# Optimization experiments

Hardware: AMD Instinct MI355X
Metric: run time of the kernel (lower is better)

Reference implementation:

```python
import jax, jax.numpy as jnp
import numpy as np

B, DIM, HEADS, H, W = 2, 256, 8, 40, 40


def setup_inputs() -> dict:
    key = jax.random.key(0)
    ks = jax.random.split(key, 11)
    s = 0.05
    return {
        "x": jax.random.normal(ks[0], (B, DIM, H, W), jnp.float32),
        "qkv_w": jax.random.normal(ks[1], (3 * DIM, DIM, 1, 1), jnp.float32) * s,
        "qkv_b": jax.random.normal(ks[2], (3 * DIM,), jnp.float32) * s,
        "pos_w": jax.random.normal(ks[3], (3 * DIM, 1, 3, 3), jnp.float32) * s,
        "pos_b": jax.random.normal(ks[4], (3 * DIM,), jnp.float32) * s,
        "proj_w": jax.random.normal(ks[5], (DIM, DIM), jnp.float32) * s,
        "proj_b": jax.random.normal(ks[6], (DIM,), jnp.float32) * s,
        "g1_w": jax.random.normal(ks[7], (16, 1), jnp.float32),
        "g1_b": jax.random.normal(ks[8], (16,), jnp.float32),
        "g2_w": jax.random.normal(ks[9], (1, 16), jnp.float32),
        "g2_b": jax.random.normal(ks[10], (1,), jnp.float32),
    }


def _conv(x, w, b, groups=1, pad=0):
    # NCHW conv, OIHW weights (matches torch Conv2d)
    y = jax.lax.conv_general_dilated(x, w, (1, 1), [(pad, pad), (pad, pad)],
                                     feature_group_count=groups)
    return y + b[None, :, None, None]


def reference(x, qkv_w, qkv_b, pos_w, pos_b, proj_w, proj_b, g1_w, g1_b, g2_w, g2_b):
    b, c, h, w = x.shape
    n = h * w
    hd = c // HEADS
    scale = hd ** -0.5

    qkv = _conv(x, qkv_w, qkv_b)                     # [b, 3c, h, w]
    qkv = _conv(qkv, pos_w, pos_b, groups=3 * c, pad=1)  # depthwise 3x3
    q, k, v = jnp.split(qkv, 3, axis=1)

    def to_heads(t):  # [b,c,h,w] -> [b, heads, n, head_dim]
        return t.reshape(b, HEADS, hd, n).transpose(0, 1, 3, 2)

    q, k, v = to_heads(q), to_heads(k), to_heads(v)

    attn = jnp.einsum('bhnd,bhmd->bhnm', q, k) * scale      # [b,H,n,n]
    prob = jax.nn.softmax(attn, axis=-1)
    entropy = -(prob * jnp.log(jnp.clip(prob, 1e-12))).sum(-1).mean(-1)  # [b,H]

    # EntropyGate: ratio in [0.1, 1.0]
    hid = jax.nn.relu(entropy[..., None] @ g1_w.T + g1_b)
    ratio = jax.nn.sigmoid(hid @ g2_w.T + g2_b)[..., 0] * 0.9 + 0.1      # [b,H]

    # dynamic per-(b,head) top-k: keep = ceil(ratio*n), clamped to [1,n]
    keep = jnp.clip(jnp.ceil(ratio * n).astype(jnp.int32), 1, n)          # [b,H]
    srt = jnp.flip(jnp.sort(attn, axis=-1), axis=-1)                      # descending
    idx = jnp.broadcast_to((keep - 1)[:, :, None, None], (b, HEADS, n, 1))
    kth = jnp.take_along_axis(srt, idx, axis=-1)                          # [b,H,n,1]
    sparse = jnp.where(attn >= kth, attn, -jnp.inf)

    p = jax.nn.softmax(sparse, axis=-1)
    out = jnp.einsum('bhnm,bhmd->bhnd', p, v)
    out = out.transpose(0, 2, 1, 3).reshape(b, n, c)
    out = out @ proj_w.T + proj_b
    return out.transpose(0, 2, 1).reshape(b, c, h, w)
```

## Files before the change

### kernel.cpp

```cpp
#include <hip/hip_runtime.h>
#include <math.h>

#define BB 2
#define CDIM 256
#define NHEADS 8
#define HD 32
#define HH 40
#define WW 40
#define NN 1600
#define C3 768
#define SCALE 0.17677669529663687f
#define RTE 8
#define RTS 2
#define TSTR 2048
#define HSTR 51200

__device__ inline unsigned fkey(float f) {
    unsigned u = __float_as_uint(f);
    return (u & 0x80000000u) ? ~u : (u | 0x80000000u);
}
__device__ inline float finv(unsigned u) {
    unsigned v = (u & 0x80000000u) ? (u ^ 0x80000000u) : ~u;
    return __uint_as_float(v);
}

__global__ __launch_bounds__(256) void conv1x1_kernel(const float* __restrict__ x,
                                                      const float* __restrict__ w,
                                                      const float* __restrict__ bias,
                                                      float* __restrict__ out) {
    int blk = blockIdx.x;
    int st = blk % 7;
    int t2 = blk / 7;
    int ocg = t2 % (C3 / 8);
    int b = t2 / (C3 / 8);
    int s = st * 256 + threadIdx.x;
    if (s >= NN) return;
    int oc0 = ocg * 8;
    const float* xb = x + (size_t)b * CDIM * NN + s;
    const float* w0 = w + (size_t)oc0 * CDIM;
    float a[8];
#pragma unroll
    for (int i = 0; i < 8; i++) a[i] = bias[oc0 + i];
#pragma unroll 4
    for (int ic = 0; ic < CDIM; ic++) {
        float xv = xb[(size_t)ic * NN];
#pragma unroll
        for (int i = 0; i < 8; i++) a[i] += w0[i * CDIM + ic] * xv;
    }
    float* ob = out + ((size_t)b * C3 + oc0) * NN + s;
#pragma unroll
    for (int i = 0; i < 8; i++) ob[(size_t)i * NN] = a[i];
}

__global__ __launch_bounds__(256) void dwconv_kernel(const float* __restrict__ in,
                                                     const float* __restrict__ w,
                                                     const float* __restrict__ bias,
                                                     float* __restrict__ out_t) {
    int idx = blockIdx.x * 256 + threadIdx.x;
    int s = idx % NN;
    int t = idx / NN;
    int c = t % C3;
    int b = t / C3;
    int y = s / WW, xx = s % WW;
    const float* ib = in + ((size_t)b * C3 + c) * NN;
    const float* wr = w + (size_t)c * 9;
    float acc = bias[c];
#pragma unroll
    for (int ky = 0; ky < 3; ky++) {
        int iy = y + ky - 1;
        if (iy < 0 || iy >= HH) continue;
#pragma unroll
        for (int kx = 0; kx < 3; kx++) {
            int ix = xx + kx - 1;
            if (ix < 0 || ix >= WW) continue;
            acc += wr[ky * 3 + kx] * ib[iy * WW + ix];
        }
    }
    int part = c >> 8;
    int r = c & 255;
    int hh = r >> 5;
    int d = r & 31;
    out_t[((size_t)(b * 3 + part) * NHEADS + hh) * HSTR + (s >> 6) * TSTR + d * 64 + (s & 63)] = acc;
}

__global__ __launch_bounds__(256) void entropy_kernel(const float* __restrict__ qkv_t,
                                                      float* __restrict__ ent) {
    int blk = blockIdx.x;
    int rt = blk % (NN / RTE);
    int bh = blk / (NN / RTE);
    int h = bh % NHEADS, b = bh / NHEADS;
    int row0 = rt * RTE;
    __shared__ float Qs[RTE][HD];
    int tid = threadIdx.x;
    const float* qt = qkv_t + ((size_t)(b * 3 + 0) * NHEADS + h) * HSTR;
    const float* ktb = qkv_t + ((size_t)(b * 3 + 1) * NHEADS + h) * HSTR;
    {
        int r = tid >> 5, d = tid & 31;
        int row = row0 + r;
        Qs[r][d] = qt[(row >> 6) * TSTR + d * 64 + (row & 63)];
    }
    __syncthreads();
    int w = tid >> 6, lane = tid & 63;
    int lr0 = 2 * w, lr1 = lr0 + 1;
    float q0[HD], q1[HD];
#pragma unroll
    for (int d = 0; d < HD; d++) { q0[d] = Qs[lr0][d]; q1[d] = Qs[lr1][d]; }
    float S0 = 0.f, T0 = 0.f, S1 = 0.f, T1 = 0.f;
#pragma unroll 1
    for (int kt = 0; kt < 25; kt++) {
        const float* kp = ktb + kt * TSTR + lane;
        float a0 = 0.f, a1 = 0.f;
#pragma unroll
        for (int dc = 0; dc < 4; dc++) {
            float kc[8];
#pragma unroll
            for (int i = 0; i < 8; i++) kc[i] = kp[(dc * 8 + i) * 64];
#pragma unroll
            for (int i = 0; i < 8; i++) {
                a0 += q0[dc * 8 + i] * kc[i];
                a1 += q1[dc * 8 + i] * kc[i];
            }
        }
        a0 *= SCALE; a1 *= SCALE;
        float e0 = __expf(a0), e1 = __expf(a1);
        S0 += e0; T0 += e0 * a0;
        S1 += e1; T1 += e1 * a1;
    }
#pragma unroll
    for (int o = 1; o < 64; o <<= 1) {
        S0 += __shfl_xor(S0, o); T0 += __shfl_xor(T0, o);
        S1 += __shfl_xor(S1, o); T1 += __shfl_xor(T1, o);
    }
    if (lane == 0) {
        ent[(size_t)bh * NN + row0 + lr0] = logf(S0) - T0 / S0;
        ent[(size_t)bh * NN + row0 + lr1] = logf(S1) - T1 / S1;
    }
}

__global__ void gate_kernel(const float* __restrict__ ent_rows,
                            const float* __restrict__ g1w, const float* __restrict__ g1b,
                            const float* __restrict__ g2w, const float* __restrict__ g2b,
                            int* __restrict__ keep) {
    int bh = blockIdx.x;
    int tid = threadIdx.x;
    __shared__ float red[4];
    float ls = 0.f;
    for (int j = tid; j < NN; j += 256) ls += ent_rows[bh * NN + j];
    for (int o = 32; o > 0; o >>= 1) ls += __shfl_down(ls, o);
    int lane = tid & 63, wid = tid >> 6;
    if (lane == 0) red[wid] = ls;
    __syncthreads();
    if (tid == 0) {
        float ent = (red[0] + red[1] + red[2] + red[3]) / (float)NN;
        float val = g2b[0];
#pragma unroll
        for (int j = 0; j < 16; j++) {
            float hid = ent * g1w[j] + g1b[j];
            if (hid < 0.f) hid = 0.f;
            val += hid * g2w[j];
        }
        float ratio = 0.9f / (1.f + expf(-val)) + 0.1f;
        int kp = (int)ceilf(ratio * (float)NN);
        if (kp < 1) kp = 1;
        if (kp > NN) kp = NN;
        keep[bh] = kp;
    }
}

__global__ __launch_bounds__(64) void sparse_attn_kernel(const float* __restrict__ qkv_t,
                                                         const int* __restrict__ keep,
                                                         float* __restrict__ oht) {
    int blk = blockIdx.x;
    int rt = blk % (NN / RTS);
    int bh = blk / (NN / RTS);
    int h = bh % NHEADS, b = bh / NHEADS;
    int row0 = rt * RTS;
    __shared__ float att[RTS][NN];
    __shared__ unsigned hist[RTS][256];
    __shared__ float Qs[RTS][HD];
    int tid = threadIdx.x;
    const float* qt = qkv_t + ((size_t)(b * 3 + 0) * NHEADS + h) * HSTR;
    const float* ktb = qkv_t + ((size_t)(b * 3 + 1) * NHEADS + h) * HSTR;
    const float* vtb = qkv_t + ((size_t)(b * 3 + 2) * NHEADS + h) * HSTR;
    {
        int r = tid >> 5, d = tid & 31;
        int row = row0 + r;
        Qs[r][d] = qt[(row >> 6) * TSTR + d * 64 + (row & 63)];
    }
    int want = keep[bh];
    __syncthreads();
    int lane = tid;
    float q0[HD], q1[HD];
#pragma unroll
    for (int d = 0; d < HD; d++) { q0[d] = Qs[0][d]; q1[d] = Qs[1][d]; }

    float m0 = -1e30f, m1 = -1e30f;
    for (int kt = 0; kt < 25; kt++) {
        const float* kp = ktb + kt * TSTR + lane;
        int j = kt * 64 + lane;
        float kc[HD];
#pragma unroll
        for (int d = 0; d < HD; d++) kc[d] = kp[d * 64];
        float a0 = 0.f, a1 = 0.f;
#pragma unroll
        for (int d = 0; d < HD; d++) { a0 += q0[d] * kc[d]; a1 += q1[d] * kc[d]; }
        a0 *= SCALE; a1 *= SCALE;
        att[0][j] = a0;
        att[1][j] = a1;
        m0 = fmaxf(m0, a0); m1 = fmaxf(m1, a1);
    }
#pragma unroll
    for (int off = 1; off < 64; off <<= 1) {
        m0 = fmaxf(m0, __shfl_xor(m0, off));
        m1 = fmaxf(m1, __shfl_xor(m1, off));
    }

    int l = lane & 31;
    int r = (lane < 32) ? 0 : 1;
    unsigned kvr[50];
#pragma unroll
    for (int k2 = 0; k2 < 50; k2++) kvr[k2] = fkey(att[r][k2 * 32 + l]);

    unsigned prefixHigh = 0;
    for (int pass = 0; pass < 4; pass++) {
        int shift = 24 - 8 * pass;
#pragma unroll
        for (int i = 0; i < 8; i++) hist[r][248 - 8 * l + i] = 0u;
#pragma unroll
        for (int k2 = 0; k2 < 50; k2++) {
            unsigned u = kvr[k2];
            bool ok = (pass == 0) || ((u >> (shift + 8)) == prefixHigh);
            if (ok) atomicAdd(&hist[r][(u >> shift) & 255u], 1u);
        }
        unsigned sch = 0;
#pragma unroll
        for (int i = 0; i < 8; i++) sch += hist[r][248 - 8 * l + i];
        unsigned inc = sch;
#pragma unroll
        for (int dlt = 1; dlt < 32; dlt <<= 1) {
            unsigned tv = __shfl_up(inc, dlt, 32);
            if (l >= dlt) inc += tv;
        }
        unsigned pref = inc - sch;
        bool found = (pref < (unsigned)want) && ((unsigned)want <= inc);
        int bsel = -1, wnew = 0;
        if (found) {
            unsigned want2 = (unsigned)want - pref, cum = 0;
#pragma unroll
            for (int i = 0; i < 8; i++) {
                int bbin = 255 - 8 * l - i;
                unsigned c = hist[r][bbin];
                if (bsel < 0 && cum + c >= want2) { bsel = bbin; wnew = (int)(want2 - cum); }
                cum += c;
            }
        }
        unsigned long long mk = __ballot(found);
        int src = (lane < 32) ? __builtin_ctzll(mk & 0xffffffffULL)
                              : __builtin_ctzll(mk >> 32) + 32;
        bsel = __shfl(bsel, src);
        want = __shfl(wnew, src);
        prefixHigh = (prefixHigh << 8) | (unsigned)bsel;
    }
    float kth = finv(prefixHigh);
    float kth0 = __shfl(kth, 0);
    float kth1 = __shfl(kth, 32);

    float acc0[HD], acc1[HD];
#pragma unroll
    for (int d = 0; d < HD; d++) { acc0[d] = 0.f; acc1[d] = 0.f; }
    float S0 = 0.f, S1 = 0.f;
    for (int kt = 0; kt < 25; kt++) {
        const float* vp = vtb + kt * TSTR + lane;
        int j = kt * 64 + lane;
        float a0 = att[0][j];
        float a1 = att[1][j];
        float p0 = (a0 >= kth0) ? __expf(a0 - m0) : 0.f;
        float p1 = (a1 >= kth1) ? __expf(a1 - m1) : 0.f;
        S0 += p0; S1 += p1;
#pragma unroll
        for (int d = 0; d < HD; d++) {
            float vv = vp[d * 64];
            acc0[d] += p0 * vv;
            acc1[d] += p1 * vv;
        }
    }
#pragma unroll
    for (int off = 1; off < 64; off <<= 1) {
        S0 += __shfl_xor(S0, off);
        S1 += __shfl_xor(S1, off);
    }

    float* scratch = &att[0][0];
    int dd = lane & 31;
    int jb = (lane < 32) ? 0 : 32;
#pragma unroll
    for (int d = 0; d < HD; d++) scratch[lane * 33 + d] = acc0[d];
    float sum0 = 0.f;
#pragma unroll
    for (int jj = 0; jj < 32; jj++) sum0 += scratch[(jb + jj) * 33 + dd];
    sum0 += __shfl_xor(sum0, 32);
#pragma unroll
    for (int d = 0; d < HD; d++) scratch[lane * 33 + d] = acc1[d];
    float sum1 = 0.f;
#pragma unroll
    for (int jj = 0; jj < 32; jj++) sum1 += scratch[(jb + jj) * 33 + dd];
    sum1 += __shfl_xor(sum1, 32);

    if (lane < 32) {
        size_t base = ((size_t)b * CDIM + h * HD + dd) * NN + row0;
        oht[base + 0] = sum0 / S0;
        oht[base + 1] = sum1 / S1;
    }
}

__global__ __launch_bounds__(256) void proj_kernel(const float* __restrict__ oht,
                                                   const float* __restrict__ pw,
                                                   const float* __restrict__ pb,
                                                   float* __restrict__ out) {
    int blk = blockIdx.x;
    int st = blk % 7;
    int t2 = blk / 7;
    int ocg = t2 % (CDIM / 8);
    int b = t2 / (CDIM / 8);
    int s = st * 256 + threadIdx.x;
    if (s >= NN) return;
    int co0 = ocg * 8;
    const float* ib = oht + (size_t)b * CDIM * NN + s;
    const float* w0 = pw + (size_t)co0 * CDIM;
    float a[8];
#pragma unroll
    for (int i = 0; i < 8; i++) a[i] = pb[co0 + i];
#pragma unroll 4
    for (int c = 0; c < CDIM; c++) {
        float xv = ib[(size_t)c * NN];
#pragma unroll
        for (int i = 0; i < 8; i++) a[i] += w0[i * CDIM + c] * xv;
    }
    float* ob = out + ((size_t)b * CDIM + co0) * NN + s;
#pragma unroll
    for (int i = 0; i < 8; i++) ob[(size_t)i * NN] = a[i];
}

extern "C" void kernel_launch(void* const* d_in, const int* in_sizes, int n_in,
                              void* d_out, int out_size, void* d_ws, size_t ws_size,
                              hipStream_t stream) {
    const float* x      = (const float*)d_in[0];
    const float* qkv_w  = (const float*)d_in[1];
    const float* qkv_b  = (const float*)d_in[2];
    const float* pos_w  = (const float*)d_in[3];
    const float* pos_b  = (const float*)d_in[4];
    const float* proj_w = (const float*)d_in[5];
    const float* proj_b = (const float*)d_in[6];
    const float* g1w    = (const float*)d_in[7];
    const float* g1b    = (const float*)d_in[8];
    const float* g2w    = (const float*)d_in[9];
    const float* g2b    = (const float*)d_in[10];
    float* out = (float*)d_out;

    float* ws   = (float*)d_ws;
    float* buf1 = ws;
    float* buf2 = buf1 + (size_t)BB * C3 * NN;
    float* ent  = buf2 + (size_t)BB * C3 * NN;
    float* oht  = ent + (size_t)BB * NHEADS * NN;
    int* keep   = (int*)(oht + (size_t)BB * CDIM * NN);

    conv1x1_kernel<<<BB * (C3 / 8) * 7, 256, 0, stream>>>(x, qkv_w, qkv_b, buf1);
    dwconv_kernel<<<BB * C3 * NN / 256, 256, 0, stream>>>(buf1, pos_w, pos_b, buf2);
    entropy_kernel<<<NHEADS * BB * (NN / RTE), 256, 0, stream>>>(buf2, ent);
    gate_kernel<<<BB * NHEADS, 256, 0, stream>>>(ent, g1w, g1b, g2w, g2b, keep);
    sparse_attn_kernel<<<NHEADS * BB * (NN / RTS), 64, 0, stream>>>(buf2, keep, oht);
    proj_kernel<<<BB * (CDIM / 8) * 7, 256, 0, stream>>>(oht, proj_w, proj_b, out);
}
```

Before: 437.4 us.

## Process four query rows per sparse-attention block with double-buffered K/V loads

Each sparse-attention block now handles four query rows instead of two, so every K and V tile loaded from global memory is reused across twice as many rows and the grid is halved. K and V tile loads are double-buffered in registers so the next tile's loads are issued while the current tile is computed. The radix top-k selection runs in two rounds over row pairs, reusing the existing histogram layout. Costs are much higher register pressure (four accumulator arrays plus two tile buffers), more shared memory per block, and lower occupancy.

```diff
diff --git a/kernel.cpp b/kernel.cpp
--- a/kernel.cpp
+++ b/kernel.cpp
@@ -11,7 +11,7 @@
 #define C3 768
 #define SCALE 0.17677669529663687f
 #define RTE 8
-#define RTS 2
+#define RTS4 4
 #define TSTR 2048
 #define HSTR 51200
 
@@ -167,127 +167,181 @@
     }
 }
 
+
+#define QKT_STEP(KT, CUR, NXT)                                                 \
+    {                                                                          \
+        int ktn = ((KT) + 1 < 25) ? (KT) + 1 : 24;                             \
+        const float* kq = ktb + ktn * TSTR + lane;                             \
+        _Pragma("unroll")                                                      \
+        for (int d = 0; d < HD; d++) NXT[d] = kq[d * 64];                      \
+        float a0 = 0.f, a1 = 0.f, a2 = 0.f, a3 = 0.f;                          \
+        _Pragma("unroll")                                                      \
+        for (int d = 0; d < HD; d++) {                                         \
+            float kv = CUR[d];                                                 \
+            a0 += q0[d] * kv; a1 += q1[d] * kv;                                \
+            a2 += q2[d] * kv; a3 += q3[d] * kv;                                \
+        }                                                                      \
+        a0 *= SCALE; a1 *= SCALE; a2 *= SCALE; a3 *= SCALE;                    \
+        int j = (KT) * 64 + lane;                                              \
+        att[0][j] = a0; att[1][j] = a1; att[2][j] = a2; att[3][j] = a3;        \
+        m0 = fmaxf(m0, a0); m1 = fmaxf(m1, a1);                                \
+        m2 = fmaxf(m2, a2); m3 = fmaxf(m3, a3);                                \
+    }
+
+#define PV_STEP(KT, CUR, NXT)                                                  \
+    {                                                                          \
+        int ktn = ((KT) + 1 < 25) ? (KT) + 1 : 24;                             \
+        const float* vq = vtb + ktn * TSTR + lane;                             \
+        _Pragma("unroll")                                                      \
+        for (int d = 0; d < HD; d++) NXT[d] = vq[d * 64];                      \
+        int j = (KT) * 64 + lane;                                              \
+        float a0 = att[0][j], a1 = att[1][j], a2 = att[2][j], a3 = att[3][j];  \
+        float p0 = (a0 >= kth0) ? __expf(a0 - m0) : 0.f;                       \
+        float p1 = (a1 >= kth1) ? __expf(a1 - m1) : 0.f;                       \
+        float p2 = (a2 >= kth2) ? __expf(a2 - m2) : 0.f;                       \
+        float p3 = (a3 >= kth3) ? __expf(a3 - m3) : 0.f;                       \
+        S0 += p0; S1 += p1; S2 += p2; S3 += p3;                                \
+        _Pragma("unroll")                                                      \
+        for (int d = 0; d < HD; d++) {                                         \
+            float vv = CUR[d];                                                 \
+            acc0[d] += p0 * vv; acc1[d] += p1 * vv;                            \
+            acc2[d] += p2 * vv; acc3[d] += p3 * vv;                            \
+        }                                                                      \
+    }
+
 __global__ __launch_bounds__(64) void sparse_attn_kernel(const float* __restrict__ qkv_t,
                                                          const int* __restrict__ keep,
                                                          float* __restrict__ oht) {
     int blk = blockIdx.x;
-    int rt = blk % (NN / RTS);
-    int bh = blk / (NN / RTS);
+    int rt = blk % (NN / RTS4);
+    int bh = blk / (NN / RTS4);
     int h = bh % NHEADS, b = bh / NHEADS;
-    int row0 = rt * RTS;
-    __shared__ float att[RTS][NN];
-    __shared__ unsigned hist[RTS][256];
-    __shared__ float Qs[RTS][HD];
+    int row0 = rt * RTS4;
+    __shared__ float att[RTS4][NN];
+    __shared__ unsigned hist[2][256];
+    __shared__ float Qs[RTS4][HD];
     int tid = threadIdx.x;
     const float* qt = qkv_t + ((size_t)(b * 3 + 0) * NHEADS + h) * HSTR;
     const float* ktb = qkv_t + ((size_t)(b * 3 + 1) * NHEADS + h) * HSTR;
     const float* vtb = qkv_t + ((size_t)(b * 3 + 2) * NHEADS + h) * HSTR;
-    {
-        int r = tid >> 5, d = tid & 31;
+#pragma unroll
+    for (int i = tid; i < RTS4 * HD; i += 64) {
+        int r = i >> 5, d = i & 31;
         int row = row0 + r;
         Qs[r][d] = qt[(row >> 6) * TSTR + d * 64 + (row & 63)];
     }
-    int want = keep[bh];
+    int want0 = keep[bh];
     __syncthreads();
     int lane = tid;
-    float q0[HD], q1[HD];
-#pragma unroll
-    for (int d = 0; d < HD; d++) { q0[d] = Qs[0][d]; q1[d] = Qs[1][d]; }
-
-    float m0 = -1e30f, m1 = -1e30f;
-    for (int kt = 0; kt < 25; kt++) {
-        const float* kp = ktb + kt * TSTR + lane;
-        int j = kt * 64 + lane;
-        float kc[HD];
-#pragma unroll
-        for (int d = 0; d < HD; d++) kc[d] = kp[d * 64];
-        float a0 = 0.f, a1 = 0.f;
-#pragma unroll
-        for (int d = 0; d < HD; d++) { a0 += q0[d] * kc[d]; a1 += q1[d] * kc[d]; }
-        a0 *= SCALE; a1 *= SCALE;
-        att[0][j] = a0;
-        att[1][j] = a1;
-        m0 = fmaxf(m0, a0); m1 = fmaxf(m1, a1);
-    }
+    float q0[HD], q1[HD], q2[HD], q3[HD];
+#pragma unroll
+    for (int d = 0; d < HD; d++) {
+        q0[d] = Qs[0][d]; q1[d] = Qs[1][d]; q2[d] = Qs[2][d]; q3[d] = Qs[3][d];
+    }
+
+    float m0 = -1e30f, m1 = -1e30f, m2 = -1e30f, m3 = -1e30f;
+    float kcA[HD], kcB[HD];
+    {
+        const float* kp0 = ktb + lane;
+#pragma unroll
+        for (int d = 0; d < HD; d++) kcA[d] = kp0[d * 64];
+    }
+#pragma unroll 1
+    for (int kt = 0; kt < 24; kt += 2) {
+        QKT_STEP(kt, kcA, kcB);
+        QKT_STEP(kt + 1, kcB, kcA);
+    }
+    QKT_STEP(24, kcA, kcB);
 #pragma unroll
     for (int off = 1; off < 64; off <<= 1) {
         m0 = fmaxf(m0, __shfl_xor(m0, off));
         m1 = fmaxf(m1, __shfl_xor(m1, off));
+        m2 = fmaxf(m2, __shfl_xor(m2, off));
+        m3 = fmaxf(m3, __shfl_xor(m3, off));
     }
 
     int l = lane & 31;
-    int r = (lane < 32) ? 0 : 1;
-    unsigned kvr[50];
-#pragma unroll
-    for (int k2 = 0; k2 < 50; k2++) kvr[k2] = fkey(att[r][k2 * 32 + l]);
-
-    unsigned prefixHigh = 0;
-    for (int pass = 0; pass < 4; pass++) {
-        int shift = 24 - 8 * pass;
-#pragma unroll
-        for (int i = 0; i < 8; i++) hist[r][248 - 8 * l + i] = 0u;
-#pragma unroll
-        for (int k2 = 0; k2 < 50; k2++) {
-            unsigned u = kvr[k2];
-            bool ok = (pass == 0) || ((u >> (shift + 8)) == prefixHigh);
-            if (ok) atomicAdd(&hist[r][(u >> shift) & 255u], 1u);
+    int r = lane >> 5;
+    float kth0, kth1, kth2, kth3;
+#pragma unroll 1
+    for (int b2 = 0; b2 < 2; b2++) {
+        int rowr = 2 * b2 + r;
+        unsigned kvr[50];
+#pragma unroll
+        for (int k2 = 0; k2 < 50; k2++) kvr[k2] = fkey(att[rowr][k2 * 32 + l]);
+        int want = want0;
+        unsigned prefixHigh = 0;
+        for (int pass = 0; pass < 4; pass++) {
+            int shift = 24 - 8 * pass;
+#pragma unroll
+            for (int i = 0; i < 8; i++) hist[r][248 - 8 * l + i] = 0u;
+#pragma unroll
+            for (int k2 = 0; k2 < 50; k2++) {
+                unsigned u = kvr[k2];
+                bool ok = (pass == 0) || ((u >> (shift + 8)) == prefixHigh);
+                if (ok) atomicAdd(&hist[r][(u >> shift) & 255u], 1u);
+            }
+            unsigned sch = 0;
+#pragma unroll
+            for (int i = 0; i < 8; i++) sch += hist[r][248 - 8 * l + i];
+            unsigned inc = sch;
+#pragma unroll
+            for (int dlt = 1; dlt < 32; dlt <<= 1) {
+                unsigned tv = __shfl_up(inc, dlt, 32);
+                if (l >= dlt) inc += tv;
+            }
+            unsigned pref = inc - sch;
+            bool found = (pref < (unsigned)want) && ((unsigned)want <= inc);
+            int bsel = -1, wnew = 0;
+            if (found) {
+                unsigned want2 = (unsigned)want - pref, cum = 0;
+#pragma unroll
+                for (int i = 0; i < 8; i++) {
+                    int bbin = 255 - 8 * l - i;
+                    unsigned c = hist[r][bbin];
+                    if (bsel < 0 && cum + c >= want2) { bsel = bbin; wnew = (int)(want2 - cum); }
+                    cum += c;
+                }
+            }
+            unsigned long long mk = __ballot(found);
+            int src = (lane < 32) ? __builtin_ctzll(mk & 0xffffffffULL)
+                                  : __builtin_ctzll(mk >> 32) + 32;
+            bsel = __shfl(bsel, src);
+            want = __shfl(wnew, src);
+            prefixHigh = (prefixHigh << 8) | (unsigned)bsel;
         }
-        unsigned sch = 0;
-#pragma unroll
-        for (int i = 0; i < 8; i++) sch += hist[r][248 - 8 * l + i];
-        unsigned inc = sch;
-#pragma unroll
-        for (int dlt = 1; dlt < 32; dlt <<= 1) {
-            unsigned tv = __shfl_up(inc, dlt, 32);
-            if (l >= dlt) inc += tv;
+        float kth = finv(prefixHigh);
+        if (b2 == 0) {
+            kth0 = __shfl(kth, 0);
+            kth1 = __shfl(kth, 32);
+        } else {
+            kth2 = __shfl(kth, 0);
+            kth3 = __shfl(kth, 32);
         }
-        unsigned pref = inc - sch;
-        bool found = (pref < (unsigned)want) && ((unsigned)want <= inc);
-        int bsel = -1, wnew = 0;
-        if (found) {
-            unsigned want2 = (unsigned)want - pref, cum = 0;
-#pragma unroll
-            for (int i = 0; i < 8; i++) {
-                int bbin = 255 - 8 * l - i;
-                unsigned c = hist[r][bbin];
-                if (bsel < 0 && cum + c >= want2) { bsel = bbin; wnew = (int)(want2 - cum); }
-                cum += c;
-            }
-        }
-        unsigned long long mk = __ballot(found);
-        int src = (lane < 32) ? __builtin_ctzll(mk & 0xffffffffULL)
-                              : __builtin_ctzll(mk >> 32) + 32;
-        bsel = __shfl(bsel, src);
-        want = __shfl(wnew, src);
-        prefixHigh = (prefixHigh << 8) | (unsigned)bsel;
-    }
-    float kth = finv(prefixHigh);
-    float kth0 = __shfl(kth, 0);
-    float kth1 = __shfl(kth, 32);
-
-    float acc0[HD], acc1[HD];
-#pragma unroll
-    for (int d = 0; d < HD; d++) { acc0[d] = 0.f; acc1[d] = 0.f; }
-    float S0 = 0.f, S1 = 0.f;
-    for (int kt = 0; kt < 25; kt++) {
-        const float* vp = vtb + kt * TSTR + lane;
-        int j = kt * 64 + lane;
-        float a0 = att[0][j];
-        float a1 = att[1][j];
-        float p0 = (a0 >= kth0) ? __expf(a0 - m0) : 0.f;
-        float p1 = (a1 >= kth1) ? __expf(a1 - m1) : 0.f;
-        S0 += p0; S1 += p1;
-#pragma unroll
-        for (int d = 0; d < HD; d++) {
-            float vv = vp[d * 64];
-            acc0[d] += p0 * vv;
-            acc1[d] += p1 * vv;
-        }
-    }
+    }
+
+    float acc0[HD], acc1[HD], acc2[HD], acc3[HD];
+#pragma unroll
+    for (int d = 0; d < HD; d++) { acc0[d] = 0.f; acc1[d] = 0.f; acc2[d] = 0.f; acc3[d] = 0.f; }
+    float S0 = 0.f, S1 = 0.f, S2 = 0.f, S3 = 0.f;
+    float vcA[HD], vcB[HD];
+    {
+        const float* vp0 = vtb + lane;
+#pragma unroll
+        for (int d = 0; d < HD; d++) vcA[d] = vp0[d * 64];
+    }
+#pragma unroll 1
+    for (int kt = 0; kt < 24; kt += 2) {
+        PV_STEP(kt, vcA, vcB);
+        PV_STEP(kt + 1, vcB, vcA);
+    }
+    PV_STEP(24, vcA, vcB);
 #pragma unroll
     for (int off = 1; off < 64; off <<= 1) {
         S0 += __shfl_xor(S0, off);
         S1 += __shfl_xor(S1, off);
+        S2 += __shfl_xor(S2, off);
+        S3 += __shfl_xor(S3, off);
     }
 
     float* scratch = &att[0][0];
@@ -305,11 +359,25 @@
 #pragma unroll
     for (int jj = 0; jj < 32; jj++) sum1 += scratch[(jb + jj) * 33 + dd];
     sum1 += __shfl_xor(sum1, 32);
+#pragma unroll
+    for (int d = 0; d < HD; d++) scratch[lane * 33 + d] = acc2[d];
+    float sum2 = 0.f;
+#pragma unroll
+    for (int jj = 0; jj < 32; jj++) sum2 += scratch[(jb + jj) * 33 + dd];
+    sum2 += __shfl_xor(sum2, 32);
+#pragma unroll
+    for (int d = 0; d < HD; d++) scratch[lane * 33 + d] = acc3[d];
+    float sum3 = 0.f;
+#pragma unroll
+    for (int jj = 0; jj < 32; jj++) sum3 += scratch[(jb + jj) * 33 + dd];
+    sum3 += __shfl_xor(sum3, 32);
 
     if (lane < 32) {
         size_t base = ((size_t)b * CDIM + h * HD + dd) * NN + row0;
         oht[base + 0] = sum0 / S0;
         oht[base + 1] = sum1 / S1;
+        oht[base + 2] = sum2 / S2;
+        oht[base + 3] = sum3 / S3;
     }
 }
 
@@ -368,6 +436,6 @@
     dwconv_kernel<<<BB * C3 * NN / 256, 256, 0, stream>>>(buf1, pos_w, pos_b, buf2);
     entropy_kernel<<<NHEADS * BB * (NN / RTE), 256, 0, stream>>>(buf2, ent);
     gate_kernel<<<BB * NHEADS, 256, 0, stream>>>(ent, g1w, g1b, g2w, g2b, keep);
-    sparse_attn_kernel<<<NHEADS * BB * (NN / RTS), 64, 0, stream>>>(buf2, keep, oht);
+    sparse_attn_kernel<<<NHEADS * BB * (NN / RTS4), 64, 0, stream>>>(buf2, keep, oht);
     proj_kernel<<<BB * (CDIM / 8) * 7, 256, 0, stream>>>(oht, proj_w, proj_b, out);
 }
```

Result: slower. 459.3 us (+5.0%).

## Store Q/K/V tiles row-major per token and prefetch K/V with double buffering

Applied to the files above, without the earlier changes.

Changes the intermediate qkv tile layout from d-major to token-major with 32 contiguous floats per token. The entropy and sparse attention kernels can then load each key or value row as eight float4 vector loads instead of 32 strided scalar loads. The QK^T and PV loops in the sparse attention kernel are software-pipelined with two register buffers so the next tile's loads are in flight during the current tile's FMAs. The trade-offs are higher register pressure, and each lane now reads a 128-byte contiguous row, so a wavefront's accesses are no longer coalesced across lanes.

```diff
diff --git a/kernel.cpp b/kernel.cpp
--- a/kernel.cpp
+++ b/kernel.cpp
@@ -14,6 +14,8 @@
 #define RTS 2
 #define TSTR 2048
 #define HSTR 51200
+
+typedef __attribute__((ext_vector_type(4))) float f4;
 
 __device__ inline unsigned fkey(float f) {
     unsigned u = __float_as_uint(f);
@@ -80,7 +82,7 @@
     int r = c & 255;
     int hh = r >> 5;
     int d = r & 31;
-    out_t[((size_t)(b * 3 + part) * NHEADS + hh) * HSTR + (s >> 6) * TSTR + d * 64 + (s & 63)] = acc;
+    out_t[((size_t)(b * 3 + part) * NHEADS + hh) * HSTR + (s >> 6) * TSTR + (s & 63) * 32 + d] = acc;
 }
 
 __global__ __launch_bounds__(256) void entropy_kernel(const float* __restrict__ qkv_t,
@@ -97,7 +99,7 @@
     {
         int r = tid >> 5, d = tid & 31;
         int row = row0 + r;
-        Qs[r][d] = qt[(row >> 6) * TSTR + d * 64 + (row & 63)];
+        Qs[r][d] = qt[(row >> 6) * TSTR + (row & 63) * 32 + d];
     }
     __syncthreads();
     int w = tid >> 6, lane = tid & 63;
@@ -108,17 +110,18 @@
     float S0 = 0.f, T0 = 0.f, S1 = 0.f, T1 = 0.f;
 #pragma unroll 1
     for (int kt = 0; kt < 25; kt++) {
-        const float* kp = ktb + kt * TSTR + lane;
+        const f4* kp = (const f4*)(ktb + kt * TSTR + lane * 32);
+        f4 kc[8];
+#pragma unroll
+        for (int i = 0; i < 8; i++) kc[i] = kp[i];
         float a0 = 0.f, a1 = 0.f;
 #pragma unroll
-        for (int dc = 0; dc < 4; dc++) {
-            float kc[8];
-#pragma unroll
-            for (int i = 0; i < 8; i++) kc[i] = kp[(dc * 8 + i) * 64];
-#pragma unroll
-            for (int i = 0; i < 8; i++) {
-                a0 += q0[dc * 8 + i] * kc[i];
-                a1 += q1[dc * 8 + i] * kc[i];
+        for (int i = 0; i < 8; i++) {
+#pragma unroll
+            for (int c = 0; c < 4; c++) {
+                float kv = kc[i][c];
+                a0 += q0[i * 4 + c] * kv;
+                a1 += q1[i * 4 + c] * kv;
             }
         }
         a0 *= SCALE; a1 *= SCALE;
@@ -166,6 +169,51 @@
         keep[bh] = kp;
     }
 }
+
+
+#define QKT_STEP(KT, CUR, NXT)                                                 \
+    {                                                                          \
+        int ktn = ((KT) + 1 < 25) ? (KT) + 1 : 24;                             \
+        const f4* kq = (const f4*)(ktb + ktn * TSTR + lane * 32);              \
+        _Pragma("unroll")                                                      \
+        for (int i = 0; i < 8; i++) NXT[i] = kq[i];                            \
+        float a0 = 0.f, a1 = 0.f;                                              \
+        _Pragma("unroll")                                                      \
+        for (int i = 0; i < 8; i++) {                                          \
+            _Pragma("unroll")                                                  \
+            for (int c = 0; c < 4; c++) {                                      \
+                float kv = CUR[i][c];                                          \
+                a0 += q0[i * 4 + c] * kv;                                      \
+                a1 += q1[i * 4 + c] * kv;                                      \
+            }                                                                  \
+        }                                                                      \
+        a0 *= SCALE; a1 *= SCALE;                                              \
+        int j = (KT) * 64 + lane;                                              \
+        att[0][j] = a0; att[1][j] = a1;                                        \
+        m0 = fmaxf(m0, a0); m1 = fmaxf(m1, a1);                                \
+    }
+
+#define PV_STEP(KT, CUR, NXT)                                                  \
+    {                                                                          \
+        int ktn = ((KT) + 1 < 25) ? (KT) + 1 : 24;                             \
+        const f4* vq = (const f4*)(vtb + ktn * TSTR + lane * 32);              \
+        _Pragma("unroll")                                                      \
+        for (int i = 0; i < 8; i++) NXT[i] = vq[i];                            \
+        int j = (KT) * 64 + lane;                                              \
+        float a0 = att[0][j], a1 = att[1][j];                                  \
+        float p0 = (a0 >= kth0) ? __expf(a0 - m0) : 0.f;                       \
+        float p1 = (a1 >= kth1) ? __expf(a1 - m1) : 0.f;                       \
+        S0 += p0; S1 += p1;                                                    \
+        _Pragma("unroll")                                                      \
+        for (int i = 0; i < 8; i++) {                                          \
+            _Pragma("unroll")                                                  \
+            for (int c = 0; c < 4; c++) {                                      \
+                float vv = CUR[i][c];                                          \
+                acc0[i * 4 + c] += p0 * vv;                                    \
+                acc1[i * 4 + c] += p1 * vv;                                    \
+            }                                                                  \
+        }                                                                      \
+    }
 
 __global__ __launch_bounds__(64) void sparse_attn_kernel(const float* __restrict__ qkv_t,
                                                          const int* __restrict__ keep,
@@ -185,7 +233,7 @@
     {
         int r = tid >> 5, d = tid & 31;
         int row = row0 + r;
-        Qs[r][d] = qt[(row >> 6) * TSTR + d * 64 + (row & 63)];
+        Qs[r][d] = qt[(row >> 6) * TSTR + (row & 63) * 32 + d];
     }
     int want = keep[bh];
     __syncthreads();
@@ -195,20 +243,18 @@
     for (int d = 0; d < HD; d++) { q0[d] = Qs[0][d]; q1[d] = Qs[1][d]; }
 
     float m0 = -1e30f, m1 = -1e30f;
-    for (int kt = 0; kt < 25; kt++) {
-        const float* kp = ktb + kt * TSTR + lane;
-        int j = kt * 64 + lane;
-        float kc[HD];
-#pragma unroll
-        for (int d = 0; d < HD; d++) kc[d] = kp[d * 64];
-        float a0 = 0.f, a1 = 0.f;
-#pragma unroll
-        for (int d = 0; d < HD; d++) { a0 += q0[d] * kc[d]; a1 += q1[d] * kc[d]; }
-        a0 *= SCALE; a1 *= SCALE;
-        att[0][j] = a0;
-        att[1][j] = a1;
-        m0 = fmaxf(m0, a0); m1 = fmaxf(m1, a1);
-    }
+    f4 kcA[8], kcB[8];
+    {
+        const f4* kp0 = (const f4*)(ktb + lane * 32);
+#pragma unroll
+        for (int i = 0; i < 8; i++) kcA[i] = kp0[i];
+    }
+#pragma unroll 1
+    for (int kt = 0; kt < 24; kt += 2) {
+        QKT_STEP(kt, kcA, kcB);
+        QKT_STEP(kt + 1, kcB, kcA);
+    }
+    QKT_STEP(24, kcA, kcB);
 #pragma unroll
     for (int off = 1; off < 64; off <<= 1) {
         m0 = fmaxf(m0, __shfl_xor(m0, off));
@@ -269,21 +315,18 @@
 #pragma unroll
     for (int d = 0; d < HD; d++) { acc0[d] = 0.f; acc1[d] = 0.f; }
     float S0 = 0.f, S1 = 0.f;
-    for (int kt = 0; kt < 25; kt++) {
-        const float* vp = vtb + kt * TSTR + lane;
-        int j = kt * 64 + lane;
-        float a0 = att[0][j];
-        float a1 = att[1][j];
-        float p0 = (a0 >= kth0) ? __expf(a0 - m0) : 0.f;
-        float p1 = (a1 >= kth1) ? __expf(a1 - m1) : 0.f;
-        S0 += p0; S1 += p1;
-#pragma unroll
-        for (int d = 0; d < HD; d++) {
-            float vv = vp[d * 64];
-            acc0[d] += p0 * vv;
-            acc1[d] += p1 * vv;
-        }
-    }
+    f4 vcA[8], vcB[8];
+    {
+        const f4* vp0 = (const f4*)(vtb + lane * 32);
+#pragma unroll
+        for (int i = 0; i < 8; i++) vcA[i] = vp0[i];
+    }
+#pragma unroll 1
+    for (int kt = 0; kt < 24; kt += 2) {
+        PV_STEP(kt, vcA, vcB);
+        PV_STEP(kt + 1, vcB, vcA);
+    }
+    PV_STEP(24, vcA, vcB);
 #pragma unroll
     for (int off = 1; off < 64; off <<= 1) {
         S0 += __shfl_xor(S0, off);
```

Result: slower. 1.027 ms (+134.9%).

## Split sparse attention block across two wavefronts with per-row radix select

Applied to the files above, without the earlier changes.

Raises the sparse attention block from one to two wavefronts. Each wave handles half of the key tiles for QK and PV, and each wave runs the 4-pass radix top-k select for one query row with 64 lanes instead of 32. Partial max, sum and accumulators are combined through shared memory with extra barriers, and the output reduction now uses shuffles before a smaller shared-memory sum. The aim is more parallelism and latency hiding per block, at the cost of extra block-level synchronisation and cross-wave reductions.

```diff
diff --git a/kernel.cpp b/kernel.cpp
--- a/kernel.cpp
+++ b/kernel.cpp
@@ -167,9 +167,9 @@
     }
 }
 
-__global__ __launch_bounds__(64) void sparse_attn_kernel(const float* __restrict__ qkv_t,
-                                                         const int* __restrict__ keep,
-                                                         float* __restrict__ oht) {
+__global__ __launch_bounds__(128) void sparse_attn_kernel(const float* __restrict__ qkv_t,
+                                                          const int* __restrict__ keep,
+                                                          float* __restrict__ oht) {
     int blk = blockIdx.x;
     int rt = blk % (NN / RTS);
     int bh = blk / (NN / RTS);
@@ -178,33 +178,46 @@
     __shared__ float att[RTS][NN];
     __shared__ unsigned hist[RTS][256];
     __shared__ float Qs[RTS][HD];
+    __shared__ float red[RTS][2];
+    __shared__ float kthS[RTS];
     int tid = threadIdx.x;
+    int wv = tid >> 6;
+    int lane = tid & 63;
     const float* qt = qkv_t + ((size_t)(b * 3 + 0) * NHEADS + h) * HSTR;
     const float* ktb = qkv_t + ((size_t)(b * 3 + 1) * NHEADS + h) * HSTR;
     const float* vtb = qkv_t + ((size_t)(b * 3 + 2) * NHEADS + h) * HSTR;
-    {
+    if (tid < 64) {
         int r = tid >> 5, d = tid & 31;
         int row = row0 + r;
         Qs[r][d] = qt[(row >> 6) * TSTR + d * 64 + (row & 63)];
     }
     int want = keep[bh];
     __syncthreads();
-    int lane = tid;
     float q0[HD], q1[HD];
 #pragma unroll
     for (int d = 0; d < HD; d++) { q0[d] = Qs[0][d]; q1[d] = Qs[1][d]; }
 
+    int t0 = wv ? 13 : 0;
+    int t1 = wv ? 25 : 13;
+
     float m0 = -1e30f, m1 = -1e30f;
-    for (int kt = 0; kt < 25; kt++) {
+#pragma unroll 1
+    for (int kt = t0; kt < t1; kt++) {
         const float* kp = ktb + kt * TSTR + lane;
+        float a0 = 0.f, a1 = 0.f;
+#pragma unroll
+        for (int dc = 0; dc < 4; dc++) {
+            float kc[8];
+#pragma unroll
+            for (int i = 0; i < 8; i++) kc[i] = kp[(dc * 8 + i) * 64];
+#pragma unroll
+            for (int i = 0; i < 8; i++) {
+                a0 += q0[dc * 8 + i] * kc[i];
+                a1 += q1[dc * 8 + i] * kc[i];
+            }
+        }
+        a0 *= SCALE; a1 *= SCALE;
         int j = kt * 64 + lane;
-        float kc[HD];
-#pragma unroll
-        for (int d = 0; d < HD; d++) kc[d] = kp[d * 64];
-        float a0 = 0.f, a1 = 0.f;
-#pragma unroll
-        for (int d = 0; d < HD; d++) { a0 += q0[d] * kc[d]; a1 += q1[d] * kc[d]; }
-        a0 *= SCALE; a1 *= SCALE;
         att[0][j] = a0;
         att[1][j] = a1;
         m0 = fmaxf(m0, a0); m1 = fmaxf(m1, a1);
@@ -214,62 +227,67 @@
         m0 = fmaxf(m0, __shfl_xor(m0, off));
         m1 = fmaxf(m1, __shfl_xor(m1, off));
     }
-
-    int l = lane & 31;
-    int r = (lane < 32) ? 0 : 1;
-    unsigned kvr[50];
-#pragma unroll
-    for (int k2 = 0; k2 < 50; k2++) kvr[k2] = fkey(att[r][k2 * 32 + l]);
-
-    unsigned prefixHigh = 0;
-    for (int pass = 0; pass < 4; pass++) {
-        int shift = 24 - 8 * pass;
-#pragma unroll
-        for (int i = 0; i < 8; i++) hist[r][248 - 8 * l + i] = 0u;
-#pragma unroll
-        for (int k2 = 0; k2 < 50; k2++) {
-            unsigned u = kvr[k2];
-            bool ok = (pass == 0) || ((u >> (shift + 8)) == prefixHigh);
-            if (ok) atomicAdd(&hist[r][(u >> shift) & 255u], 1u);
-        }
-        unsigned sch = 0;
-#pragma unroll
-        for (int i = 0; i < 8; i++) sch += hist[r][248 - 8 * l + i];
-        unsigned inc = sch;
-#pragma unroll
-        for (int dlt = 1; dlt < 32; dlt <<= 1) {
-            unsigned tv = __shfl_up(inc, dlt, 32);
-            if (l >= dlt) inc += tv;
-        }
-        unsigned pref = inc - sch;
-        bool found = (pref < (unsigned)want) && ((unsigned)want <= inc);
-        int bsel = -1, wnew = 0;
-        if (found) {
-            unsigned want2 = (unsigned)want - pref, cum = 0;
-#pragma unroll
-            for (int i = 0; i < 8; i++) {
-                int bbin = 255 - 8 * l - i;
-                unsigned c = hist[r][bbin];
-                if (bsel < 0 && cum + c >= want2) { bsel = bbin; wnew = (int)(want2 - cum); }
-                cum += c;
+    if (lane == 0) { red[0][wv] = m0; red[1][wv] = m1; }
+    __syncthreads();
+    m0 = fmaxf(red[0][0], red[0][1]);
+    m1 = fmaxf(red[1][0], red[1][1]);
+
+    {
+        int r = wv;
+        unsigned kvr[25];
+#pragma unroll
+        for (int k2 = 0; k2 < 25; k2++) kvr[k2] = fkey(att[r][k2 * 64 + lane]);
+        unsigned prefixHigh = 0;
+        for (int pass = 0; pass < 4; pass++) {
+            int shift = 24 - 8 * pass;
+#pragma unroll
+            for (int i = 0; i < 4; i++) hist[r][252 - 4 * lane + i] = 0u;
+#pragma unroll
+            for (int k2 = 0; k2 < 25; k2++) {
+                unsigned u = kvr[k2];
+                bool ok = (pass == 0) || ((u >> (shift + 8)) == prefixHigh);
+                if (ok) atomicAdd(&hist[r][(u >> shift) & 255u], 1u);
             }
-        }
-        unsigned long long mk = __ballot(found);
-        int src = (lane < 32) ? __builtin_ctzll(mk & 0xffffffffULL)
-                              : __builtin_ctzll(mk >> 32) + 32;
-        bsel = __shfl(bsel, src);
-        want = __shfl(wnew, src);
-        prefixHigh = (prefixHigh << 8) | (unsigned)bsel;
-    }
-    float kth = finv(prefixHigh);
-    float kth0 = __shfl(kth, 0);
-    float kth1 = __shfl(kth, 32);
+            unsigned sch = 0;
+#pragma unroll
+            for (int i = 0; i < 4; i++) sch += hist[r][252 - 4 * lane + i];
+            unsigned inc = sch;
+#pragma unroll
+            for (int dlt = 1; dlt < 64; dlt <<= 1) {
+                unsigned tv = __shfl_up(inc, dlt, 64);
+                if (lane >= dlt) inc += tv;
+            }
+            unsigned pref = inc - sch;
+            bool found = (pref < (unsigned)want) && ((unsigned)want <= inc);
+            int bsel = -1, wnew = 0;
+            if (found) {
+                unsigned want2 = (unsigned)want - pref, cum = 0;
+#pragma unroll
+                for (int i = 0; i < 4; i++) {
+                    int bbin = 255 - 4 * lane - i;
+                    unsigned c = hist[r][bbin];
+                    if (bsel < 0 && cum + c >= want2) { bsel = bbin; wnew = (int)(want2 - cum); }
+                    cum += c;
+                }
+            }
+            unsigned long long mk = __ballot(found);
+            int src = __builtin_ctzll(mk);
+            bsel = __shfl(bsel, src);
+            want = __shfl(wnew, src);
+            prefixHigh = (prefixHigh << 8) | (unsigned)bsel;
+        }
+        if (lane == 0) kthS[r] = finv(prefixHigh);
+    }
+    __syncthreads();
+    float kth0 = kthS[0];
+    float kth1 = kthS[1];
 
     float acc0[HD], acc1[HD];
 #pragma unroll
     for (int d = 0; d < HD; d++) { acc0[d] = 0.f; acc1[d] = 0.f; }
     float S0 = 0.f, S1 = 0.f;
-    for (int kt = 0; kt < 25; kt++) {
+#pragma unroll 1
+    for (int kt = t0; kt < t1; kt++) {
         const float* vp = vtb + kt * TSTR + lane;
         int j = kt * 64 + lane;
         float a0 = att[0][j];
@@ -289,27 +307,39 @@
         S0 += __shfl_xor(S0, off);
         S1 += __shfl_xor(S1, off);
     }
-
-    float* scratch = &att[0][0];
-    int dd = lane & 31;
-    int jb = (lane < 32) ? 0 : 32;
-#pragma unroll
-    for (int d = 0; d < HD; d++) scratch[lane * 33 + d] = acc0[d];
-    float sum0 = 0.f;
-#pragma unroll
-    for (int jj = 0; jj < 32; jj++) sum0 += scratch[(jb + jj) * 33 + dd];
-    sum0 += __shfl_xor(sum0, 32);
-#pragma unroll
-    for (int d = 0; d < HD; d++) scratch[lane * 33 + d] = acc1[d];
-    float sum1 = 0.f;
-#pragma unroll
-    for (int jj = 0; jj < 32; jj++) sum1 += scratch[(jb + jj) * 33 + dd];
-    sum1 += __shfl_xor(sum1, 32);
-
-    if (lane < 32) {
-        size_t base = ((size_t)b * CDIM + h * HD + dd) * NN + row0;
-        oht[base + 0] = sum0 / S0;
-        oht[base + 1] = sum1 / S1;
+    if (lane == 0) { red[0][wv] = S0; red[1][wv] = S1; }
+
+#pragma unroll
+    for (int d = 0; d < HD; d++) {
+        acc0[d] += __shfl_xor(acc0[d], 32);
+        acc1[d] += __shfl_xor(acc1[d], 32);
+        acc0[d] += __shfl_xor(acc0[d], 16);
+        acc1[d] += __shfl_xor(acc1[d], 16);
+    }
+    __syncthreads();
+    float* sc = &att[0][0];
+    {
+        int idx = lane & 15;
+        if (lane < 16) {
+#pragma unroll
+            for (int d = 0; d < HD; d++) sc[((wv * 2 + 0) * 16 + idx) * 33 + d] = acc0[d];
+        } else if (lane < 32) {
+#pragma unroll
+            for (int d = 0; d < HD; d++) sc[((wv * 2 + 1) * 16 + idx) * 33 + d] = acc1[d];
+        }
+    }
+    __syncthreads();
+    if (wv == 0) {
+        int row = lane >> 5;
+        int d = lane & 31;
+        float s = 0.f;
+#pragma unroll
+        for (int w2 = 0; w2 < 2; w2++)
+#pragma unroll
+            for (int i = 0; i < 16; i++)
+                s += sc[((w2 * 2 + row) * 16 + i) * 33 + d];
+        float Srow = red[row][0] + red[row][1];
+        oht[((size_t)b * CDIM + h * HD + d) * NN + row0 + row] = s / Srow;
     }
 }
 
@@ -368,6 +398,6 @@
     dwconv_kernel<<<BB * C3 * NN / 256, 256, 0, stream>>>(buf1, pos_w, pos_b, buf2);
     entropy_kernel<<<NHEADS * BB * (NN / RTE), 256, 0, stream>>>(buf2, ent);
     gate_kernel<<<BB * NHEADS, 256, 0, stream>>>(ent, g1w, g1b, g2w, g2b, keep);
-    sparse_attn_kernel<<<NHEADS * BB * (NN / RTS), 64, 0, stream>>>(buf2, keep, oht);
+    sparse_attn_kernel<<<NHEADS * BB * (NN / RTS), 128, 0, stream>>>(buf2, keep, oht);
     proj_kernel<<<BB * (CDIM / 8) * 7, 256, 0, stream>>>(oht, proj_w, proj_b, out);
 }
```

After: 457.4 us. +4.6%, slower.
